# Kernel tuning notes

Hardware: AMD Instinct MI355X
Metric: run time of the kernel (lower is better)

## Reference

```python
import jax, jax.numpy as jnp
import numpy as np

B, L, DM = 4, 2048, 1024  # batch, seq len (== l_max, global kernel), d_model; head_dim = 1


def setup_inputs() -> dict:
    key = jax.random.key(0)
    ks = jax.random.split(key, 13)
    n = lambda k, shape, s=1.0: jax.random.normal(k, shape, dtype=jnp.float32) * s
    W_SCALE = 0.02   # keeps activations well-conditioned through the chained convs
    K_SCALE = 0.02
    return {
        "u": n(ks[0], (B, L, DM)),
        "Wq": n(ks[1], (DM, DM), W_SCALE), "bq": n(ks[2], (DM,), W_SCALE),
        "Wk": n(ks[3], (DM, DM), W_SCALE), "bk": n(ks[4], (DM,), W_SCALE),
        "Wv": n(ks[5], (DM, DM), W_SCALE), "bv": n(ks[6], (DM,), W_SCALE),
        "k_kernel": n(ks[7], (DM, L), K_SCALE),
        "k_D": n(ks[8], (DM,)),
        "ssm_kernel": n(ks[9], (DM, L), K_SCALE),
        "D": n(ks[10], (DM,)),
        "Wo": n(ks[11], (DM, DM), W_SCALE), "bo": n(ks[12], (DM,), W_SCALE),
    }


def reference(u, Wq, bq, Wk, bk, Wv, bv, k_kernel, k_D, ssm_kernel, D, Wo, bo):
    # u: (B, L, H) with H = d_model (head_dim = 1)
    Lseq = u.shape[1]
    fft_size = 2 * Lseq  # zero-pad to 2L for linear (causal) convolution

    # q/k/v projections -> (B, H, L)
    q = jnp.einsum('blh,dh->bdl', u, Wq) + bq[None, :, None]
    k = jnp.einsum('blh,dh->bdl', u, Wk) + bk[None, :, None]
    v = jnp.einsum('blh,dh->bdl', u, Wv) + bv[None, :, None]

    # shift conv on k: k <- k_kernel * k (causal FFT conv) + k_D * k
    k_kernel_f = jnp.fft.rfft(k_kernel, n=fft_size)           # (H, F)
    k_f = jnp.fft.rfft(k, n=fft_size)                          # (B, H, F)
    shift_k = jnp.fft.irfft(k_kernel_f[None] * k_f, n=fft_size)[..., :Lseq]
    k = shift_k + k_D[None, :, None] * k

    # head_dim == 1: kv outer product collapses to elementwise gate
    kv = k * v                                                 # (B, H, L)

    # ssm conv on kv (torch's 1/fft_size + norm='forward' irfft == standard irfft)
    kv_f = jnp.fft.rfft(kv, n=fft_size)                        # (B, H, F)
    ssm_kernel_f = jnp.fft.rfft(ssm_kernel, n=fft_size)        # (H, F)
    y = jnp.fft.irfft(kv_f * ssm_kernel_f[None], n=fft_size)[..., :Lseq]
    y = y + kv * D[None, :, None]                              # D skip

    # q gating, then output projection
    y = y * q                                                  # (B, H, L)
    y = jnp.swapaxes(y, 1, 2)                                  # (B, L, H)
    return jnp.einsum('blh,oh->blo', y, Wo) + bo
```

## Files before the change

### kernel.cpp

```cpp
#include <hip/hip_runtime.h>
#include <hip/hip_bf16.h>
#include <stdint.h>

#define DM   1024
#define LSEQ 2048
#define NB   4

typedef __attribute__((ext_vector_type(8))) short  short8;
typedef __attribute__((ext_vector_type(4))) float  floatx4;

__device__ __forceinline__ ushort f2b(float x) {
    union { float f; uint32_t u; } v; v.f = x;
    uint32_t b = v.u + 0x7FFF + ((v.u >> 16) & 1);
    return (ushort)(b >> 16);
}
__device__ __forceinline__ float b2f(ushort x) {
    union { uint32_t u; float f; } v; v.u = ((uint32_t)x) << 16;
    return v.f;
}

__global__ __launch_bounds__(256) void cvt_bf16_kernel(const float* __restrict__ in,
                                                       ushort* __restrict__ out, int n8) {
    int i = blockIdx.x * 256 + threadIdx.x;
    if (i >= n8) return;
    const float4* p = (const float4*)in + (size_t)i * 2;
    float4 a = p[0], b = p[1];
    union { ushort us[8]; uint4 v; } o;
    o.us[0] = f2b(a.x); o.us[1] = f2b(a.y); o.us[2] = f2b(a.z); o.us[3] = f2b(a.w);
    o.us[4] = f2b(b.x); o.us[5] = f2b(b.y); o.us[6] = f2b(b.z); o.us[7] = f2b(b.w);
    ((uint4*)out)[i] = o.v;
}

__global__ __launch_bounds__(256) void cvt_w_kernel(const float* __restrict__ Wq,
                                                    const float* __restrict__ Wk,
                                                    const float* __restrict__ Wv,
                                                    const float* __restrict__ Wo,
                                                    ushort* __restrict__ dst) {
    const int per = DM * DM / 8;
    int i = blockIdx.x * 256 + threadIdx.x;
    int r = i / per;
    const float* src = (r == 0) ? Wq : (r == 1) ? Wk : (r == 2) ? Wv : Wo;
    int j = i - r * per;
    const float4* p = (const float4*)src + (size_t)j * 2;
    float4 a = p[0], b = p[1];
    union { ushort us[8]; uint4 v; } o;
    o.us[0] = f2b(a.x); o.us[1] = f2b(a.y); o.us[2] = f2b(a.z); o.us[3] = f2b(a.w);
    o.us[4] = f2b(b.x); o.us[5] = f2b(b.y); o.us[6] = f2b(b.z); o.us[7] = f2b(b.w);
    ((uint4*)dst)[i] = o.v;
}

template <int MODE>
__global__ __launch_bounds__(512, 2) void gemm_bt2(const ushort* __restrict__ Aw,
                                                   const ushort* __restrict__ Bw,
                                                   const float* __restrict__ b0,
                                                   const float* __restrict__ b1,
                                                   const float* __restrict__ b2,
                                                   void* __restrict__ C0v,
                                                   void* __restrict__ C1v,
                                                   void* __restrict__ C2v,
                                                   int M, int N, int K, int nbx) {
    constexpr int BM = 128, BN = 256, BK = 64;
    constexpr int BUFB = 49152;
    __shared__ char lds[3 * BUFB];

    const int tid   = threadIdx.x;
    const int wave  = tid >> 6;
    const int lane  = tid & 63;
    const int qlane = lane & 15;
    const int qk    = lane >> 4;

    int flat = blockIdx.y * nbx + blockIdx.x;
    int nwg  = nbx * gridDim.y;
    int swz  = (flat & 7) * (nwg >> 3) + (flat >> 3);
    const int tn = (swz % nbx) * BN;
    const int tm = (swz / nbx) * BM;

    const int wmo = (wave >> 2) * 64;
    const int wno = (wave & 3) * 64;
    const int NT  = K / BK;

#define STAGE(kt, p)                                                                          \
    {                                                                                         \
        const int k0_ = (kt) * BK;                                                            \
        char* Ab_ = lds + (p) * BUFB;                                                         \
        char* Bb_ = Ab_ + 16384;                                                              \
        _Pragma("unroll")                                                                     \
        for (int j = 0; j < 2; ++j) {                                                         \
            int id = wave * 64 + lane + j * 512;                                              \
            int row = id >> 3, s = id & 7;                                                    \
            const ushort* src = Aw + (size_t)(tm + row) * K + k0_ + ((s ^ (row & 7)) * 8);    \
            __builtin_amdgcn_global_load_lds((const __attribute__((address_space(1))) void*)src, \
                (__attribute__((address_space(3))) void*)(Ab_ + wave * 1024 + j * 8192), 16, 0, 0); \
        }                                                                                     \
        _Pragma("unroll")                                                                     \
        for (int j = 0; j < 4; ++j) {                                                         \
            int id = wave * 64 + lane + j * 512;                                              \
            int row = id >> 3, s = id & 7;                                                    \
            const ushort* src = Bw + (size_t)(tn + row) * K + k0_ + ((s ^ (row & 7)) * 8);    \
            __builtin_amdgcn_global_load_lds((const __attribute__((address_space(1))) void*)src, \
                (__attribute__((address_space(3))) void*)(Bb_ + wave * 1024 + j * 8192), 16, 0, 0); \
        }                                                                                     \
    }

    floatx4 acc[4][4] = {};

    STAGE(0, 0);
    STAGE(1, 1);

    const int z7 = qlane & 7;

    for (int t = 0; t < NT; ++t) {
        const int cur = t % 3;
        if (t < NT - 1) asm volatile("s_waitcnt vmcnt(6)" ::: "memory");
        else            asm volatile("s_waitcnt vmcnt(0)" ::: "memory");
        __builtin_amdgcn_s_barrier();
        __builtin_amdgcn_sched_barrier(0);

        if (t + 2 < NT) STAGE(t + 2, (t + 2) % 3);

        const char* Ab = lds + cur * BUFB;
        const char* Bb = Ab + 16384;
#pragma unroll
        for (int kk = 0; kk < 2; ++kk) {
            const int slot = ((kk * 4 + qk) ^ z7) << 4;
            short8 af[4], bfv[4];
#pragma unroll
            for (int i = 0; i < 4; ++i) {
                int r = wmo + i * 16 + qlane;
                af[i] = *(const short8*)(Ab + r * 128 + slot);
            }
#pragma unroll
            for (int j = 0; j < 4; ++j) {
                int r = wno + j * 16 + qlane;
                bfv[j] = *(const short8*)(Bb + r * 128 + slot);
            }
            __builtin_amdgcn_s_setprio(1);
#pragma unroll
            for (int i = 0; i < 4; ++i)
#pragma unroll
                for (int j = 0; j < 4; ++j)
                    acc[i][j] = __builtin_amdgcn_mfma_f32_16x16x32_bf16(af[i], bfv[j], acc[i][j], 0, 0, 0);
            __builtin_amdgcn_s_setprio(0);
        }
    }
#undef STAGE

#pragma unroll
    for (int i = 0; i < 4; ++i) {
#pragma unroll
        for (int j = 0; j < 4; ++j) {
            int n  = tn + wno + j * 16 + qlane;
            int m0 = tm + wmo + i * 16 + qk * 4;
            if (MODE == 0) {
                int proj = n >> 10, dd = n & (DM - 1);
                const float* bb = (proj == 0) ? b0 : (proj == 1) ? b1 : b2;
                ushort* Cb      = (ushort*)((proj == 0) ? C0v : (proj == 1) ? C1v : C2v);
                float bv = bb[dd];
                int b = m0 >> 11, l = m0 & (LSEQ - 1);
                ushort4 val;
                val.x = f2b(acc[i][j][0] + bv);
                val.y = f2b(acc[i][j][1] + bv);
                val.z = f2b(acc[i][j][2] + bv);
                val.w = f2b(acc[i][j][3] + bv);
                *(ushort4*)(Cb + ((size_t)b * DM + dd) * LSEQ + l) = val;
            } else {
                float* C0 = (float*)C0v;
                float bv = b0[n];
#pragma unroll
                for (int r = 0; r < 4; ++r)
                    C0[(size_t)(m0 + r) * N + n] = acc[i][j][r] + bv;
            }
        }
    }
}

#define KSTR 2096
#define XSTR 2248

__global__ __launch_bounds__(512) void conv_mfma_kernel(const ushort* __restrict__ x,
                                                        const float* __restrict__ ker,
                                                        const float* __restrict__ scale,
                                                        const ushort* __restrict__ gate,
                                                        ushort* __restrict__ out) {
    __shared__ ushort krev[KSTR];
    __shared__ ushort xs[4 * XSTR];
    const int d    = blockIdx.x;
    const int tid  = threadIdx.x;
    const int wave = tid >> 6;
    const int lane = tid & 63;

    {
        int b = wave >> 1, half = wave & 1;
        const ushort* src = x + ((size_t)b * DM + d) * LSEQ + half * 1024 + lane * 8;
        char* dst = (char*)xs + b * (XSTR * 2) + 256 + half * 2048;
#pragma unroll
        for (int c = 0; c < 2; ++c)
            __builtin_amdgcn_global_load_lds((const __attribute__((address_space(1))) void*)(src + c * 512),
                                             (__attribute__((address_space(3))) void*)(dst + c * 1024),
                                             16, 0, 0);
    }
    {
        const float* krow = ker + (size_t)d * LSEQ;
        int e0 = tid * 4;
        float4 kv = *(const float4*)(krow + e0);
        ushort4 o;
        o.x = f2b(kv.w); o.y = f2b(kv.z); o.z = f2b(kv.y); o.w = f2b(kv.x);
        *(ushort4*)(krev + (2060 - e0)) = o;
        uint4 z = {0, 0, 0, 0};
        if (tid < 2)  *(uint4*)((char*)krev + tid * 16) = z;
        if (tid >= 2 && tid < 6) *(uint4*)((char*)krev + 4128 + (tid - 2) * 16) = z;
        if (tid >= 64 && tid < 128) {
            int b = (tid - 64) >> 4, c = (tid - 64) & 15;
            *(uint4*)((char*)xs + b * (XSTR * 2) + c * 16) = z;
        }
        if (tid >= 128 && tid < 144) {
            int b = (tid - 128) >> 2, c = (tid - 128) & 3;
            *(uint4*)((char*)xs + b * (XSTR * 2) + 4352 + c * 16) = z;
        }
    }
    __syncthreads();

    const int qn = lane & 15;
    const int qk = lane >> 4;

    int g[2] = {wave, 15 - wave};
    const int smax_all = 128 * (15 - wave) + 128;

    const int lbase = (qn & 3) * XSTR + 128 + 16 * (qn >> 2) + 8 * qk;

    floatx4 acc[2][2] = {};

    short8 fE[2], fO[2];
#pragma unroll
    for (int gi = 0; gi < 2; ++gi) {
        fE[gi] = *(const short8*)(xs + lbase + 128 * g[gi] + 64);
        fO[gi] = *(const short8*)(xs + lbase + 128 * g[gi] + 32);
    }

#define CSTEP(SS, FP)                                                                        \
    {                                                                                        \
        int b_el = 2063 - qn + 8 * qk - (SS);                                                \
        int A0 = b_el & ~3;                                                                  \
        uint2 w0 = *(const uint2*)(krev + A0);                                               \
        uint2 w1 = *(const uint2*)(krev + A0 + 4);                                           \
        uint2 w2 = *(const uint2*)(krev + A0 + 8);                                           \
        int qsel = (b_el >> 1) & 1;                                                          \
        uint sh  = (uint)(b_el & 1) * 16u;                                                   \
        uint e0 = qsel ? w0.y : w0.x;                                                        \
        uint e1 = qsel ? w1.x : w0.y;                                                        \
        uint e2 = qsel ? w1.y : w1.x;                                                        \
        uint e3 = qsel ? w2.x : w1.y;                                                        \
        uint e4 = qsel ? w2.y : w2.x;                                                        \
        union { uint u[4]; short8 v; } Af;                                                   \
        Af.u[0] = __builtin_amdgcn_alignbit(e1, e0, sh);                                     \
        Af.u[1] = __builtin_amdgcn_alignbit(e2, e1, sh);                                     \
        Af.u[2] = __builtin_amdgcn_alignbit(e3, e2, sh);                                     \
        Af.u[3] = __builtin_amdgcn_alignbit(e4, e3, sh);                                     \
        _Pragma("unroll")                                                                    \
        for (int gi = 0; gi < 2; ++gi) {                                                     \
            if ((SS) <= 128 * g[gi] + 128) {                                                 \
                short8 fN = *(const short8*)(xs + lbase + 128 * g[gi] - (SS));               \
                acc[gi][0] = __builtin_amdgcn_mfma_f32_16x16x32_bf16(Af.v, fN, acc[gi][0], 0, 0, 0); \
                acc[gi][1] = __builtin_amdgcn_mfma_f32_16x16x32_bf16(Af.v, FP[gi], acc[gi][1], 0, 0, 0); \
                FP[gi] = fN;                                                                 \
            }                                                                                \
        }                                                                                    \
    }

    for (int s = 0; s <= smax_all; s += 64) {
        CSTEP(s, fE);
        if (s + 32 <= smax_all) CSTEP(s + 32, fO);
    }
#undef CSTEP

    const float sc = scale[d];
#pragma unroll
    for (int gi = 0; gi < 2; ++gi) {
#pragma unroll
        for (int m = 0; m < 2; ++m) {
            int p  = 8 * g[gi] + 4 * m + (qn >> 2);
            int b  = qn & 3;
            int l0 = 16 * p + 4 * qk;
            size_t off = ((size_t)b * DM + d) * LSEQ + l0;
            ushort4 xv = *(const ushort4*)(xs + b * XSTR + 128 + l0);
            ushort4 gv = *(const ushort4*)(gate + off);
            ushort4 ov;
            ov.x = f2b((acc[gi][m][0] + sc * b2f(xv.x)) * b2f(gv.x));
            ov.y = f2b((acc[gi][m][1] + sc * b2f(xv.y)) * b2f(gv.y));
            ov.z = f2b((acc[gi][m][2] + sc * b2f(xv.z)) * b2f(gv.z));
            ov.w = f2b((acc[gi][m][3] + sc * b2f(xv.w)) * b2f(gv.w));
            *(ushort4*)(out + off) = ov;
        }
    }
}

__global__ __launch_bounds__(256) void transpose_bf16(const ushort* __restrict__ in,
                                                      ushort* __restrict__ out) {
    __shared__ ushort t[32][36];
    const int l0 = blockIdx.x * 32;
    const int d0 = blockIdx.y * 32;
    const int b  = blockIdx.z;
    const int q  = threadIdx.x & 7;
    const int r  = threadIdx.x >> 3;
    *(ushort4*)(&t[r][q * 4]) = *(const ushort4*)(in + ((size_t)b * DM + d0 + r) * LSEQ + l0 + q * 4);
    __syncthreads();
    ushort4 o;
    o.x = t[q * 4 + 0][r]; o.y = t[q * 4 + 1][r]; o.z = t[q * 4 + 2][r]; o.w = t[q * 4 + 3][r];
    *(ushort4*)(out + ((size_t)b * LSEQ + l0 + r) * DM + d0 + q * 4) = o;
}

extern "C" void kernel_launch(void* const* d_in, const int* in_sizes, int n_in,
                              void* d_out, int out_size, void* d_ws, size_t ws_size,
                              hipStream_t stream) {
    const float* u        = (const float*)d_in[0];
    const float* Wq       = (const float*)d_in[1];
    const float* bq       = (const float*)d_in[2];
    const float* Wk       = (const float*)d_in[3];
    const float* bk       = (const float*)d_in[4];
    const float* Wv       = (const float*)d_in[5];
    const float* bv       = (const float*)d_in[6];
    const float* k_kernel = (const float*)d_in[7];
    const float* k_D      = (const float*)d_in[8];
    const float* ssm_ker  = (const float*)d_in[9];
    const float* Dv       = (const float*)d_in[10];
    const float* Wo       = (const float*)d_in[11];
    const float* bo       = (const float*)d_in[12];
    float* outp = (float*)d_out;

    char* ws = (char*)d_ws;
    ushort* Q    = (ushort*)(ws);
    ushort* KV   = (ushort*)(ws + (16ull << 20));
    ushort* V    = (ushort*)(ws + (32ull << 20));
    ushort* U16  = (ushort*)(ws + (48ull << 20));
    ushort* YT   = (ushort*)(ws + (64ull << 20));
    ushort* Wcat = (ushort*)(ws + (80ull << 20));

    cvt_bf16_kernel<<<(NB * LSEQ * DM / 8) / 256, 256, 0, stream>>>(u, U16, NB * LSEQ * DM / 8);
    cvt_w_kernel<<<(4 * DM * DM / 8) / 256, 256, 0, stream>>>(Wq, Wk, Wv, Wo, Wcat);

    dim3 g1(3 * DM / 256, NB * LSEQ / 128);
    gemm_bt2<0><<<g1, 512, 0, stream>>>(U16, Wcat, bq, bk, bv, Q, KV, V,
                                        NB * LSEQ, 3 * DM, DM, 3 * DM / 256);

    conv_mfma_kernel<<<DM, 512, 0, stream>>>(KV, k_kernel, k_D, V, KV);
    conv_mfma_kernel<<<DM, 512, 0, stream>>>(KV, ssm_ker, Dv, Q, KV);

    dim3 g2(LSEQ / 32, DM / 32, NB);
    transpose_bf16<<<g2, 256, 0, stream>>>(KV, YT);

    dim3 g3(DM / 256, NB * LSEQ / 128);
    gemm_bt2<1><<<g3, 512, 0, stream>>>(YT, Wcat + 3 * DM * DM, bo, bo, bo,
                                        outp, outp, outp, NB * LSEQ, DM, DM, DM / 256);
}
```

Before: 172.2 us.

## Add 256x256-tile ping-pong GEMM for the fused QKV projection

Result: no change. 173.2 us (+0.6%).

```diff
diff --git a/kernel.cpp b/kernel.cpp
--- a/kernel.cpp
+++ b/kernel.cpp
@@ -47,6 +47,160 @@
     o.us[0] = f2b(a.x); o.us[1] = f2b(a.y); o.us[2] = f2b(a.z); o.us[3] = f2b(a.w);
     o.us[4] = f2b(b.x); o.us[5] = f2b(b.y); o.us[6] = f2b(b.z); o.us[7] = f2b(b.w);
     ((uint4*)dst)[i] = o.v;
+}
+
+template <int MODE>
+__global__ __launch_bounds__(512, 2) void gemm_8p(const ushort* __restrict__ Aw,
+                                                  const ushort* __restrict__ Bw,
+                                                  const float* __restrict__ b0,
+                                                  const float* __restrict__ b1,
+                                                  const float* __restrict__ b2,
+                                                  void* __restrict__ C0v,
+                                                  void* __restrict__ C1v,
+                                                  void* __restrict__ C2v,
+                                                  int N, int nbx) {
+    constexpr int K = 1024, BK = 64, NT = K / BK;
+    __shared__ char lds[131072];
+
+    const int tid   = threadIdx.x;
+    const int wave  = tid >> 6;
+    const int lane  = tid & 63;
+    const int qlane = lane & 15;
+    const int qk    = lane >> 4;
+    const int z7    = qlane & 7;
+    const int wm    = wave >> 2;
+    const int wn    = wave & 3;
+
+    int flat = blockIdx.y * nbx + blockIdx.x;
+    int nwg  = nbx * gridDim.y;
+    int swz  = (flat & 7) * (nwg >> 3) + (flat >> 3);
+    const int tn = (swz % nbx) * 256;
+    const int tm = (swz / nbx) * 256;
+
+    const int srcChunkOff   = (((lane & 7) ^ (lane >> 3)) * 8);
+    const int srcRowInSlice = (lane >> 3);
+
+#define STAGE_H(TT, ISB, H)                                                                   \
+    {                                                                                         \
+        const ushort* gbase = (ISB) ? Bw : Aw;                                                \
+        const int trow = ((ISB) ? tn : tm) + (H) * 128 + wave * 16 + srcRowInSlice;           \
+        char* dst = lds + ((ISB) ? 65536 : 0) + ((((TT) & 1) * 2 + (H)) * 16384) + wave * 2048; \
+        const int k0_ = (TT) * BK;                                                            \
+        _Pragma("unroll")                                                                     \
+        for (int j = 0; j < 2; ++j) {                                                         \
+            const ushort* src = gbase + (size_t)(trow + j * 8) * K + k0_ + srcChunkOff;       \
+            __builtin_amdgcn_global_load_lds(                                                 \
+                (const __attribute__((address_space(1))) void*)src,                           \
+                (__attribute__((address_space(3))) void*)(dst + j * 1024), 16, 0, 0);         \
+        }                                                                                     \
+    }
+
+    short8 af[4][2], bf0[2][2], bf1[2][2];
+    floatx4 acc[2][2][4][2] = {};
+
+#define LDA(TT, MH)                                                                           \
+    {                                                                                         \
+        const char* Ab = lds + ((((TT) & 1) * 2 + (MH)) * 16384);                             \
+        _Pragma("unroll")                                                                     \
+        for (int i = 0; i < 4; ++i) {                                                         \
+            int lr = wm * 64 + i * 16 + qlane;                                                \
+            _Pragma("unroll")                                                                 \
+            for (int ks = 0; ks < 2; ++ks)                                                    \
+                af[i][ks] = *(const short8*)(Ab + lr * 128 + (((ks * 4 + qk) ^ z7) << 4));    \
+        }                                                                                     \
+    }
+#define LDB(TT, NH, BF)                                                                       \
+    {                                                                                         \
+        const char* Bb = lds + 65536 + ((((TT) & 1) * 2 + (NH)) * 16384);                     \
+        _Pragma("unroll")                                                                     \
+        for (int j = 0; j < 2; ++j) {                                                         \
+            int lr = wn * 32 + j * 16 + qlane;                                                \
+            _Pragma("unroll")                                                                 \
+            for (int ks = 0; ks < 2; ++ks)                                                    \
+                BF[j][ks] = *(const short8*)(Bb + lr * 128 + (((ks * 4 + qk) ^ z7) << 4));    \
+        }                                                                                     \
+    }
+#define MFMAQ(MH, NH, BF)                                                                     \
+    __builtin_amdgcn_s_setprio(1);                                                           \
+    _Pragma("unroll")                                                                         \
+    for (int ks = 0; ks < 2; ++ks)                                                            \
+        _Pragma("unroll")                                                                     \
+        for (int i = 0; i < 4; ++i)                                                           \
+            _Pragma("unroll")                                                                 \
+            for (int j = 0; j < 2; ++j)                                                       \
+                acc[MH][NH][i][j] = __builtin_amdgcn_mfma_f32_16x16x32_bf16(                  \
+                    af[i][ks], BF[j][ks], acc[MH][NH][i][j], 0, 0, 0);                        \
+    __builtin_amdgcn_s_setprio(0);
+#define BAR  __builtin_amdgcn_s_barrier(); __builtin_amdgcn_sched_barrier(0)
+#define LGKM0 asm volatile("s_waitcnt lgkmcnt(0)" ::: "memory"); __builtin_amdgcn_sched_barrier(0)
+
+    STAGE_H(0, 0, 0); STAGE_H(0, 1, 0); STAGE_H(0, 1, 1); STAGE_H(0, 0, 1);
+    STAGE_H(1, 0, 0); STAGE_H(1, 1, 0); STAGE_H(1, 1, 1);
+    asm volatile("s_waitcnt vmcnt(6)" ::: "memory");
+    __builtin_amdgcn_s_barrier();
+    __builtin_amdgcn_sched_barrier(0);
+
+    for (int t = 0; t < NT; ++t) {
+        LDA(t, 0);
+        LDB(t, 0, bf0);
+        if (t + 1 < NT) STAGE_H(t + 1, 0, 1);
+        BAR; LGKM0;
+        MFMAQ(0, 0, bf0);
+        BAR;
+        LDB(t, 1, bf1);
+        if (t + 2 < NT) STAGE_H(t + 2, 0, 0);
+        BAR; LGKM0;
+        MFMAQ(0, 1, bf1);
+        BAR;
+        LDA(t, 1);
+        if (t + 2 < NT) STAGE_H(t + 2, 1, 0);
+        BAR; LGKM0;
+        MFMAQ(1, 0, bf0);
+        BAR;
+        if (t + 2 < NT) STAGE_H(t + 2, 1, 1);
+        if (t + 2 < NT)      { asm volatile("s_waitcnt vmcnt(6)" ::: "memory"); }
+        else if (t + 1 < NT) { asm volatile("s_waitcnt vmcnt(0)" ::: "memory"); }
+        BAR; LGKM0;
+        MFMAQ(1, 1, bf1);
+        BAR;
+    }
+#undef STAGE_H
+#undef LDA
+#undef LDB
+#undef MFMAQ
+#undef BAR
+#undef LGKM0
+
+#pragma unroll
+    for (int mh = 0; mh < 2; ++mh)
+#pragma unroll
+    for (int nh = 0; nh < 2; ++nh)
+#pragma unroll
+    for (int i = 0; i < 4; ++i)
+#pragma unroll
+    for (int j = 0; j < 2; ++j) {
+        int n  = tn + nh * 128 + wn * 32 + j * 16 + qlane;
+        int m0 = tm + mh * 128 + wm * 64 + i * 16 + qk * 4;
+        if (MODE == 0) {
+            int proj = n >> 10, dd = n & (DM - 1);
+            const float* bb = (proj == 0) ? b0 : (proj == 1) ? b1 : b2;
+            ushort* Cb      = (ushort*)((proj == 0) ? C0v : (proj == 1) ? C1v : C2v);
+            float bv = bb[dd];
+            int b = m0 >> 11, l = m0 & (LSEQ - 1);
+            ushort4 val;
+            val.x = f2b(acc[mh][nh][i][j][0] + bv);
+            val.y = f2b(acc[mh][nh][i][j][1] + bv);
+            val.z = f2b(acc[mh][nh][i][j][2] + bv);
+            val.w = f2b(acc[mh][nh][i][j][3] + bv);
+            *(ushort4*)(Cb + ((size_t)b * DM + dd) * LSEQ + l) = val;
+        } else {
+            float* C0 = (float*)C0v;
+            float bv = b0[n];
+#pragma unroll
+            for (int r = 0; r < 4; ++r)
+                C0[(size_t)(m0 + r) * N + n] = acc[mh][nh][i][j][r] + bv;
+        }
+    }
 }
 
 template <int MODE>
@@ -338,9 +492,9 @@
     cvt_bf16_kernel<<<(NB * LSEQ * DM / 8) / 256, 256, 0, stream>>>(u, U16, NB * LSEQ * DM / 8);
     cvt_w_kernel<<<(4 * DM * DM / 8) / 256, 256, 0, stream>>>(Wq, Wk, Wv, Wo, Wcat);
 
-    dim3 g1(3 * DM / 256, NB * LSEQ / 128);
-    gemm_bt2<0><<<g1, 512, 0, stream>>>(U16, Wcat, bq, bk, bv, Q, KV, V,
-                                        NB * LSEQ, 3 * DM, DM, 3 * DM / 256);
+    dim3 g1(3 * DM / 256, NB * LSEQ / 256);
+    gemm_8p<0><<<g1, 512, 0, stream>>>(U16, Wcat, bq, bk, bv, Q, KV, V,
+                                       3 * DM, 3 * DM / 256);
 
     conv_mfma_kernel<<<DM, 512, 0, stream>>>(KV, k_kernel, k_D, V, KV);
     conv_mfma_kernel<<<DM, 512, 0, stream>>>(KV, ssm_ker, Dv, Q, KV);
```
